# Kernel tuning notes

Hardware: AMD Instinct MI355X
Metric: run time of the kernel (lower is better)

The kernel has to match this reference:

```python
import jax, jax.numpy as jnp
import numpy as np

N = 100000        # nodes
E_HALF = 800000   # random edges before symmetrization
HID = 128         # hidden_dim
K = 4             # Chebyshev order
NEG = 0.01        # leaky_relu negative slope
BN_EPS = 1e-5
L2_EPS = 1e-12


def setup_inputs() -> dict:
    key = jax.random.key(0)
    ks = jax.random.split(key, 4)
    x = jax.random.normal(ks[0], (N, 3), dtype=jnp.float32)
    e = jax.random.randint(ks[1], (2, E_HALF), 0, N, dtype=jnp.int32)
    # symmetrize so the sym-normalized Laplacian is well defined
    edge_index = jnp.concatenate([e, e[::-1]], axis=1).astype(jnp.int64)

    def wcheb(k, fin, fout):
        return jax.random.normal(k, (K, fin, fout), dtype=jnp.float32) * np.float32(1.0 / np.sqrt(fin * K))

    wk = jax.random.split(ks[2], 5)
    return {
        "x": x, "edge_index": edge_index,
        "W1": wcheb(wk[0], 3, HID),   "b1": jnp.zeros((HID,), jnp.float32),
        "W2": wcheb(wk[1], HID, HID), "b2": jnp.zeros((HID,), jnp.float32),
        "W3": wcheb(wk[2], HID, HID), "b3": jnp.zeros((HID,), jnp.float32),
        "W4": wcheb(wk[3], HID, HID), "b4": jnp.zeros((HID,), jnp.float32),
        "g1": jnp.ones((HID,), jnp.float32), "be1": jnp.zeros((HID,), jnp.float32),
        "g2": jnp.ones((HID,), jnp.float32), "be2": jnp.zeros((HID,), jnp.float32),
        "g3": jnp.ones((HID,), jnp.float32), "be3": jnp.zeros((HID,), jnp.float32),
        "Wrep": jax.random.normal(wk[4], (HID, 3), dtype=jnp.float32) * np.float32(1.0 / np.sqrt(HID)),
        "brep": jnp.zeros((3,), jnp.float32),
    }


def _cheb(x, src, dst, norm, W, b):
    """PyG ChebConv (sym norm, lambda_max=2): out = sum_k T_k(L_hat) x @ W_k + b."""
    def prop(t):  # (L_hat t)_i = sum_{e: src->dst==i} norm_e * t[src_e]
        return jax.ops.segment_sum(t[src] * norm[:, None], dst, num_segments=N)
    Tx0 = x
    out = Tx0 @ W[0]
    Tx1 = prop(Tx0)
    out = out + Tx1 @ W[1]
    for k in range(2, W.shape[0]):
        Tx2 = 2.0 * prop(Tx1) - Tx0
        out = out + Tx2 @ W[k]
        Tx0, Tx1 = Tx1, Tx2
    return out + b


def _bn(x, g, b):  # BatchNorm1d, training mode (batch stats, biased var)
    mu = x.mean(axis=0)
    var = ((x - mu) ** 2).mean(axis=0)
    return (x - mu) * jax.lax.rsqrt(var + BN_EPS) * g + b


def _leaky(x):
    return jnp.where(x >= 0, x, NEG * x)


def reference(x, edge_index, W1, b1, W2, b2, W3, b3, W4, b4,
              g1, be1, g2, be2, g3, be3, Wrep, brep):
    src, dst = edge_index[0], edge_index[1]
    deg = jax.ops.segment_sum(jnp.ones(src.shape, jnp.float32), src, num_segments=N)
    dinv = jnp.where(deg > 0, jax.lax.rsqrt(jnp.maximum(deg, 1.0)), 0.0)
    # scaled Laplacian L_hat = -D^{-1/2} A D^{-1/2} (zero diagonal) for lambda_max=2
    norm = -(dinv[src] * dinv[dst])  # [E]

    h = _cheb(x.astype(jnp.float32), src, dst, norm, W1, b1)
    h = _bn(_leaky(h), g1, be1)
    h = _cheb(h, src, dst, norm, W2, b2)
    h = _bn(_leaky(h), g2, be2)
    h = _cheb(h, src, dst, norm, W3, b3)
    h = _bn(jnp.maximum(h, 0.0), g3, be3)
    h = _cheb(h, src, dst, norm, W4, b4)
    h = h / jnp.maximum(jnp.linalg.norm(h, axis=1, keepdims=True), L2_EPS)
    return h @ Wrep + brep  # [N, 3]
```

## Files before the change

### kernel.cpp

```cpp
#include <hip/hip_runtime.h>
#include <hip/hip_bf16.h>


#define HID 128
#define NEG 0.01f
#define BN_EPS 1e-5f
#define L2_EPS 1e-12f
#define CAP 64

typedef __attribute__((ext_vector_type(8))) short short8;
typedef __attribute__((ext_vector_type(4))) float floatx4;

__device__ __forceinline__ short f2bf(float f) {
    unsigned u = __float_as_uint(f);
    return (short)((u + 0x7fffu + ((u >> 16) & 1u)) >> 16);
}
__device__ __forceinline__ unsigned pack2bf(float x, float y) {
    return (unsigned)(unsigned short)f2bf(x) | ((unsigned)(unsigned short)f2bf(y) << 16);
}
__device__ __forceinline__ float bflo(unsigned u) { return __uint_as_float(u << 16); }
__device__ __forceinline__ float bfhi(unsigned u) { return __uint_as_float(u & 0xffff0000u); }
__device__ __forceinline__ float bf2f(unsigned short h) { return __uint_as_float((unsigned)h << 16); }

__device__ __forceinline__ float actf(float v, int act) {
    if (act == 0) return v >= 0.f ? v : NEG * v;
    if (act == 1) return v > 0.f ? v : 0.f;
    return v;
}


__global__ __launch_bounds__(256) void k_zero(int* __restrict__ arr, float* __restrict__ S, int N) {
    int i = blockIdx.x * 256 + threadIdx.x;
    if (i < N) arr[i * CAP] = 0;
    if (blockIdx.x == 0) {
        for (int k = threadIdx.x; k < 1024; k += 256) S[k] = 0.f;
    }
}

__global__ __launch_bounds__(256) void k_fillpad(const int* __restrict__ src, const int* __restrict__ dst,
                                                 int* __restrict__ arr, int E) {
    int e = blockIdx.x * 256 + threadIdx.x;
    if (e >= E) return;
    int d = dst[e];
    int pos = atomicAdd(&arr[d * CAP], 1);
    if (pos < CAP - 1) arr[d * CAP + 1 + pos] = src[e];
}

__global__ __launch_bounds__(256) void k_dinv(const int* __restrict__ arr, float* __restrict__ dinv,
                                              int* __restrict__ cnt, int N) {
    int i = blockIdx.x * 256 + threadIdx.x;
    if (i < N) {
        int d = arr[i * CAP];
        dinv[i] = d > 0 ? rsqrtf((float)d) : 0.f;
        cnt[i] = d < CAP - 1 ? d : CAP - 1;
    }
}

__global__ __launch_bounds__(256) void k_norm(const int* __restrict__ arr, const int* __restrict__ cnt,
                                              const float* __restrict__ dinv, int2* __restrict__ edges,
                                              float* __restrict__ snorm, int N) {
    int node = blockIdx.x * 4 + (threadIdx.x >> 6);
    if (node >= N) return;
    node = __builtin_amdgcn_readfirstlane(node);
    int lane = threadIdx.x & 63;
    int deg = cnt[node];
    float dd = dinv[node];
    int s = (lane < deg) ? arr[node * CAP + 1 + lane] : 0;
    float w = (lane < deg) ? -(dinv[s] * dd) : 0.f;
    if (lane < deg) {
        int2 rec;
        rec.x = s;
        rec.y = __float_as_int(w);
        edges[node * CAP + lane] = rec;
    }
    float sw = w;
    #pragma unroll
    for (int d = 1; d < 64; d <<= 1) sw += __shfl_xor(sw, d);
    if (lane == 0) snorm[node] = sw;
}


__global__ __launch_bounds__(256) void k_prop3(const float* __restrict__ T, const float* __restrict__ prev,
                                               float* __restrict__ out, const int* __restrict__ cnt,
                                               const int2* __restrict__ edges,
                                               float a, float b, int N) {
    int i = blockIdx.x * 256 + threadIdx.x;
    if (i >= N) return;
    float a0 = 0.f, a1 = 0.f, a2 = 0.f;
    int deg = cnt[i];
    int base = i * CAP;
    for (int j = 0; j < deg; ++j) {
        int2 r = edges[base + j];
        float w = __int_as_float(r.y);
        a0 += w * T[r.x * 3 + 0];
        a1 += w * T[r.x * 3 + 1];
        a2 += w * T[r.x * 3 + 2];
    }
    float r0 = a * a0, r1 = a * a1, r2 = a * a2;
    if (prev) {
        r0 += b * prev[i * 3 + 0];
        r1 += b * prev[i * 3 + 1];
        r2 += b * prev[i * 3 + 2];
    }
    out[i * 3 + 0] = r0;
    out[i * 3 + 1] = r1;
    out[i * 3 + 2] = r2;
}

__global__ __launch_bounds__(256, 8) void k_prop1(const unsigned* __restrict__ OUT,
                                                  unsigned* __restrict__ T1, unsigned* __restrict__ T0,
                                                  const int* __restrict__ cnt, const int2* __restrict__ edges,
                                                  const float* __restrict__ snorm, const float* __restrict__ S,
                                                  const float* __restrict__ g, const float* __restrict__ be,
                                                  int act, float invN, int N) {
    int lane = threadIdx.x & 63;
    int f0 = 2 * lane;
    float mu0 = S[f0] * invN, mu1 = S[f0 + 1] * invN;
    float v0 = S[f0 + 128] * invN - mu0 * mu0;
    float v1 = S[f0 + 129] * invN - mu1 * mu1;
    float a0 = g[f0] * rsqrtf(v0 + BN_EPS), a1 = g[f0 + 1] * rsqrtf(v1 + BN_EPS);
    float c0 = be[f0] - mu0 * a0, c1 = be[f0 + 1] - mu1 * a1;

    int wv = blockIdx.x * 4 + (threadIdx.x >> 6);
    int stride = gridDim.x * 4;
    for (int nv = wv; nv < N; nv += stride) {
        int node = __builtin_amdgcn_readfirstlane(nv);
        int deg = cnt[node];
        const int2* eb = edges + (size_t)node * CAP;
        float accx = 0.f, accy = 0.f;
        int j = 0;
        int nb = deg >> 3;
        if (nb > 0) {
            int2 recA[8]; unsigned tA[8];
            int2 recB[8]; unsigned tB[8];
            #pragma unroll
            for (int k = 0; k < 8; ++k) recA[k] = eb[k];
            #pragma unroll
            for (int k = 0; k < 8; ++k) tA[k] = OUT[(size_t)recA[k].x * 64 + lane];
            for (int bi = 1; bi < nb; ++bi) {
                const int2* ebb = eb + bi * 8;
                #pragma unroll
                for (int k = 0; k < 8; ++k) recB[k] = ebb[k];
                #pragma unroll
                for (int k = 0; k < 8; ++k) tB[k] = OUT[(size_t)recB[k].x * 64 + lane];
                #pragma unroll
                for (int k = 0; k < 8; ++k) {
                    float w = __int_as_float(recA[k].y);
                    accx += w * actf(bflo(tA[k]), act);
                    accy += w * actf(bfhi(tA[k]), act);
                }
                #pragma unroll
                for (int k = 0; k < 8; ++k) { recA[k] = recB[k]; tA[k] = tB[k]; }
            }
            #pragma unroll
            for (int k = 0; k < 8; ++k) {
                float w = __int_as_float(recA[k].y);
                accx += w * actf(bflo(tA[k]), act);
                accy += w * actf(bfhi(tA[k]), act);
            }
            j = nb * 8;
        }
        for (; j < deg; ++j) {
            int2 r = eb[j];
            float w = __int_as_float(r.y);
            unsigned t0 = OUT[(size_t)r.x * 64 + lane];
            accx += w * actf(bflo(t0), act);
            accy += w * actf(bfhi(t0), act);
        }
        float si = snorm[node];
        __builtin_nontemporal_store(pack2bf(a0 * accx + si * c0, a1 * accy + si * c1),
                                    &T1[(size_t)node * 64 + lane]);
        unsigned h = OUT[(size_t)node * 64 + lane];
        float t0lo = a0 * actf(bflo(h), act) + c0;
        float t0hi = a1 * actf(bfhi(h), act) + c1;
        __builtin_nontemporal_store(pack2bf(t0lo, t0hi), &T0[(size_t)node * 64 + lane]);
    }
}

__global__ __launch_bounds__(256, 8) void k_prop128(const unsigned* __restrict__ T, const unsigned* __restrict__ prev,
                                                    unsigned* __restrict__ out, const int* __restrict__ cnt,
                                                    const int2* __restrict__ edges,
                                                    float a, float b, int N) {
    int lane = threadIdx.x & 63;
    int wv = blockIdx.x * 4 + (threadIdx.x >> 6);
    int stride = gridDim.x * 4;
    for (int nv = wv; nv < N; nv += stride) {
        int node = __builtin_amdgcn_readfirstlane(nv);
        int deg = cnt[node];
        const int2* eb = edges + (size_t)node * CAP;
        float accx = 0.f, accy = 0.f;
        int j = 0;
        int nb = deg >> 3;
        if (nb > 0) {
            int2 recA[8]; unsigned tA[8];
            int2 recB[8]; unsigned tB[8];
            #pragma unroll
            for (int k = 0; k < 8; ++k) recA[k] = eb[k];
            #pragma unroll
            for (int k = 0; k < 8; ++k) tA[k] = T[(size_t)recA[k].x * 64 + lane];
            for (int bi = 1; bi < nb; ++bi) {
                const int2* ebb = eb + bi * 8;
                #pragma unroll
                for (int k = 0; k < 8; ++k) recB[k] = ebb[k];
                #pragma unroll
                for (int k = 0; k < 8; ++k) tB[k] = T[(size_t)recB[k].x * 64 + lane];
                #pragma unroll
                for (int k = 0; k < 8; ++k) {
                    float w = __int_as_float(recA[k].y);
                    accx += w * bflo(tA[k]);
                    accy += w * bfhi(tA[k]);
                }
                #pragma unroll
                for (int k = 0; k < 8; ++k) { recA[k] = recB[k]; tA[k] = tB[k]; }
            }
            #pragma unroll
            for (int k = 0; k < 8; ++k) {
                float w = __int_as_float(recA[k].y);
                accx += w * bflo(tA[k]);
                accy += w * bfhi(tA[k]);
            }
            j = nb * 8;
        }
        for (; j < deg; ++j) {
            int2 r = eb[j];
            float w = __int_as_float(r.y);
            unsigned t0 = T[(size_t)r.x * 64 + lane];
            accx += w * bflo(t0);
            accy += w * bfhi(t0);
        }
        float rx = a * accx, ry = a * accy;
        if (prev) {
            unsigned p = __builtin_nontemporal_load(&prev[(size_t)node * 64 + lane]);
            rx += b * bflo(p);
            ry += b * bfhi(p);
        }
        __builtin_nontemporal_store(pack2bf(rx, ry), &out[(size_t)node * 64 + lane]);
    }
}


__global__ __launch_bounds__(256) void k_gemm1(const float* __restrict__ x, const float* __restrict__ t1,
                                               const float* __restrict__ t2, const float* __restrict__ t3,
                                               const float* __restrict__ W, const float* __restrict__ b,
                                               unsigned short* __restrict__ OUT, float* __restrict__ S,
                                               int npb, int N) {
    __shared__ float Wl[12 * 128];
    __shared__ float bl[128];
    __shared__ float sS[256];
    int tid = threadIdx.x;
    for (int i = tid; i < 1536; i += 256) Wl[i] = W[i];
    if (tid < 128) bl[tid] = b[tid];
    if (tid < 256) sS[tid] = 0.f;
    __syncthreads();
    int f = tid & 127;
    int base = blockIdx.x * npb;
    int end = base + npb < N ? base + npb : N;
    const float* rows[4] = {x, t1, t2, t3};
    float s1 = 0.f, s2 = 0.f;
    for (int node = base + (tid >> 7); node < end; node += 2) {
        float acc = bl[f];
        #pragma unroll
        for (int k = 0; k < 4; ++k) {
            const float* r = rows[k] + (size_t)node * 3;
            acc += r[0] * Wl[(k * 3 + 0) * 128 + f];
            acc += r[1] * Wl[(k * 3 + 1) * 128 + f];
            acc += r[2] * Wl[(k * 3 + 2) * 128 + f];
        }
        unsigned short h = (unsigned short)f2bf(acc);
        OUT[(size_t)node * 128 + f] = h;
        float u = actf(bf2f(h), 0);
        s1 += u;
        s2 += u * u;
    }
    atomicAdd(&sS[f], s1);
    atomicAdd(&sS[f + 128], s2);
    __syncthreads();
    if (tid < 256) atomicAdd(&S[tid], sS[tid]);
}


__global__ __launch_bounds__(256) void k_packW(const float* __restrict__ WA, const float* __restrict__ WB,
                                               const float* __restrict__ WC, short* __restrict__ Wp) {
    int gid = blockIdx.x * 256 + threadIdx.x;
    int L = gid >> 16;
    int idx = gid & 65535;
    int j = idx & 7;
    int lane = (idx >> 3) & 63;
    int rest = idx >> 9;
    int nt = rest & 7;
    int ks = rest >> 3;
    int kk = ks * 32 + (lane >> 4) * 8 + j;
    int c = nt * 16 + (lane & 15);
    const float* W = (L == 0) ? WA : (L == 1) ? WB : WC;
    Wp[gid] = f2bf(W[(size_t)(kk >> 7) * 16384 + (kk & 127) * 128 + c]);
}

__global__ __launch_bounds__(512) void k_gemm512(const short* __restrict__ T0, const short* __restrict__ T1,
                                                 const short* __restrict__ T2, const short* __restrict__ T3,
                                                 const short* __restrict__ Wp, const float* __restrict__ bias,
                                                 unsigned short* __restrict__ OUT, float* __restrict__ S,
                                                 const float* __restrict__ Wrep, const float* __restrict__ brep,
                                                 float* __restrict__ fout,
                                                 int M, int doStats, int doFinal, int act) {
    __shared__ short Wlds[65536];
    __shared__ float sS[256];
    __shared__ float sW[388];
    int tid = threadIdx.x;
    int lane = tid & 63, wave = tid >> 6;
    if (tid < 256) sS[tid] = 0.f;
    if (doFinal) {
        for (int i = tid; i < 384; i += 512) sW[i] = Wrep[i];
        if (tid < 3) sW[384 + tid] = brep[tid];
    }
    for (int i = tid; i < 8192; i += 512) ((int4*)Wlds)[i] = ((const int4*)Wp)[i];
    __syncthreads();

    int quad = lane >> 4;
    int col0 = lane & 15;
    const short* Ts[4] = {T0, T1, T2, T3};
    float s1[8], s2[8];
    #pragma unroll
    for (int i = 0; i < 8; ++i) { s1[i] = 0.f; s2[i] = 0.f; }

    int nt32 = (M + 31) / 32;
    int stride = gridDim.x * 8;
    for (int t = blockIdx.x * 8 + wave; t < nt32; t += stride) {
        int r0 = t * 32;
        int rowa = r0 + col0;
        int rowb = rowa + 16;
        size_t rb0 = (size_t)(rowa < M ? rowa : M - 1) * 128;
        size_t rb1 = (size_t)(rowb < M ? rowb : M - 1) * 128;
        floatx4 acc0[8], acc1[8];
        #pragma unroll
        for (int i = 0; i < 8; ++i) {
            acc0[i][0] = 0.f; acc0[i][1] = 0.f; acc0[i][2] = 0.f; acc0[i][3] = 0.f;
            acc1[i][0] = 0.f; acc1[i][1] = 0.f; acc1[i][2] = 0.f; acc1[i][3] = 0.f;
        }
        #pragma unroll 4
        for (int ks = 0; ks < 16; ++ks) {
            const short* Tm = Ts[ks >> 2];
            int aoff = (ks & 3) * 32 + quad * 8;
            short8 af0 = *((const short8*)(Tm + rb0 + aoff));
            short8 af1 = *((const short8*)(Tm + rb1 + aoff));
            #pragma unroll
            for (int nt = 0; nt < 8; ++nt) {
                short8 bf = *((const short8*)(Wlds + ((ks * 8 + nt) * 64 + lane) * 8));
                acc0[nt] = __builtin_amdgcn_mfma_f32_16x16x32_bf16(af0, bf, acc0[nt], 0, 0, 0);
                acc1[nt] = __builtin_amdgcn_mfma_f32_16x16x32_bf16(af1, bf, acc1[nt], 0, 0, 0);
            }
        }
        if (doFinal) {
            #pragma unroll
            for (int half = 0; half < 2; ++half) {
                #pragma unroll
                for (int rg = 0; rg < 4; ++rg) {
                    int r = r0 + half * 16 + quad * 4 + rg;
                    float sq = 0.f, p0 = 0.f, p1 = 0.f, p2 = 0.f;
                    #pragma unroll
                    for (int nt = 0; nt < 8; ++nt) {
                        int c = nt * 16 + col0;
                        float v = (half ? acc1[nt][rg] : acc0[nt][rg]) + bias[c];
                        sq += v * v;
                        p0 += v * sW[c * 3 + 0];
                        p1 += v * sW[c * 3 + 1];
                        p2 += v * sW[c * 3 + 2];
                    }
                    #pragma unroll
                    for (int d = 1; d < 16; d <<= 1) {
                        sq += __shfl_xor(sq, d);
                        p0 += __shfl_xor(p0, d);
                        p1 += __shfl_xor(p1, d);
                        p2 += __shfl_xor(p2, d);
                    }
                    if (col0 == 0 && r < M) {
                        float inv = 1.f / fmaxf(sqrtf(sq), L2_EPS);
                        fout[r * 3 + 0] = p0 * inv + sW[384];
                        fout[r * 3 + 1] = p1 * inv + sW[385];
                        fout[r * 3 + 2] = p2 * inv + sW[386];
                    }
                }
            }
        } else {
            #pragma unroll
            for (int half = 0; half < 2; ++half) {
                int rbase = r0 + half * 16 + quad * 4;
                #pragma unroll
                for (int nt = 0; nt < 8; ++nt) {
                    int c = nt * 16 + col0;
                    float bv = bias[c];
                    #pragma unroll
                    for (int rg = 0; rg < 4; ++rg) {
                        int r = rbase + rg;
                        if (r < M) {
                            float v = (half ? acc1[nt][rg] : acc0[nt][rg]) + bv;
                            unsigned short h = (unsigned short)f2bf(v);
                            OUT[(size_t)r * 128 + c] = h;
                            float u = actf(bf2f(h), act);
                            s1[nt] += u;
                            s2[nt] += u * u;
                        }
                    }
                }
            }
        }
    }
    if (doStats) {
        #pragma unroll
        for (int nt = 0; nt < 8; ++nt) {
            int c = nt * 16 + col0;
            atomicAdd(&sS[c], s1[nt]);
            atomicAdd(&sS[c + 128], s2[nt]);
        }
        __syncthreads();
        if (tid < 256) atomicAdd(&S[tid], sS[tid]);
    }
}


extern "C" void kernel_launch(void* const* d_in, const int* in_sizes, int n_in,
                              void* d_out, int out_size, void* d_ws, size_t ws_size,
                              hipStream_t stream) {
    const int N = in_sizes[0] / 3;
    const int E = in_sizes[1] / 2;

    const float* x    = (const float*)d_in[0];
    const int*   ei   = (const int*)d_in[1];
    const int* esrc = ei;
    const int* edst = ei + E;
    const float* W1 = (const float*)d_in[2];  const float* b1 = (const float*)d_in[3];
    const float* W2 = (const float*)d_in[4];  const float* b2 = (const float*)d_in[5];
    const float* W3 = (const float*)d_in[6];  const float* b3 = (const float*)d_in[7];
    const float* W4 = (const float*)d_in[8];  const float* b4 = (const float*)d_in[9];
    const float* g1 = (const float*)d_in[10]; const float* be1 = (const float*)d_in[11];
    const float* g2 = (const float*)d_in[12]; const float* be2 = (const float*)d_in[13];
    const float* g3 = (const float*)d_in[14]; const float* be3 = (const float*)d_in[15];
    const float* Wrep = (const float*)d_in[16]; const float* brep = (const float*)d_in[17];
    float* out = (float*)d_out;

    char* w = (char*)d_ws;
    size_t off = 0;
    auto alloc = [&](size_t bytes) { size_t o = off; off = (off + bytes + 255) & ~(size_t)255; return o; };
    int*   arr    = (int*)(w + alloc((size_t)N * CAP * 4));
    int*   cnt    = (int*)(w + alloc((size_t)N * 4));
    float* dinv   = (float*)(w + alloc((size_t)N * 4));
    float* snorm  = (float*)(w + alloc((size_t)N * 4));
    int2*  edges  = (int2*)(w + alloc((size_t)N * CAP * 8));
    short* Wp     = (short*)(w + alloc(3 * 65536 * 2));
    float* S      = (float*)(w + alloc(4 * 256 * 4));
    float* t1f    = (float*)(w + alloc((size_t)N * 3 * 4));
    float* t2f    = (float*)(w + alloc((size_t)N * 3 * 4));
    float* t3f    = (float*)(w + alloc((size_t)N * 3 * 4));
    short* T0     = (short*)(w + alloc((size_t)N * 128 * 2));
    short* T1     = (short*)(w + alloc((size_t)N * 128 * 2));
    short* T2     = (short*)(w + alloc((size_t)N * 128 * 2));
    short* T3     = (short*)(w + alloc((size_t)N * 128 * 2));
    unsigned short* OUT = (unsigned short*)(w + alloc((size_t)N * 128 * 2));

    int gE = (E + 255) / 256;
    int gN = (N + 255) / 256;
    int gW = (N + 3) / 4;
    int gP = 2048;
    float invN = 1.f / (float)N;
    int npb = (N + 255) / 256;

    k_zero<<<gN, 256, 0, stream>>>(arr, S, N);
    k_fillpad<<<gE, 256, 0, stream>>>(esrc, edst, arr, E);
    k_dinv<<<gN, 256, 0, stream>>>(arr, dinv, cnt, N);
    k_norm<<<gW, 256, 0, stream>>>(arr, cnt, dinv, edges, snorm, N);
    k_packW<<<768, 256, 0, stream>>>(W2, W3, W4, Wp);

    k_prop3<<<gN, 256, 0, stream>>>(x, nullptr, t1f, cnt, edges, 1.f, 0.f, N);
    k_prop3<<<gN, 256, 0, stream>>>(t1f, x, t2f, cnt, edges, 2.f, -1.f, N);
    k_prop3<<<gN, 256, 0, stream>>>(t2f, t1f, t3f, cnt, edges, 2.f, -1.f, N);
    k_gemm1<<<256, 256, 0, stream>>>(x, t1f, t2f, t3f, W1, b1, OUT, S, npb, N);

    const float* bs[3]  = {b2, b3, b4};
    const float* gs[3]  = {g2, g3, nullptr};
    const float* bes[3] = {be2, be3, nullptr};
    int actsIn[3] = {0, 0, 1};
    int actsOut[3] = {0, 1, 2};

    for (int l = 0; l < 3; ++l) {
        float* Sin = S + (size_t)l * 256;
        float* Sout = S + (size_t)(l + 1) * 256;
        const float* gc = (l == 0) ? g1 : gs[l - 1];
        const float* bc = (l == 0) ? be1 : bes[l - 1];
        k_prop1<<<gP, 256, 0, stream>>>((const unsigned*)OUT, (unsigned*)T1, (unsigned*)T0,
                                        cnt, edges, snorm, Sin, gc, bc, actsIn[l], invN, N);
        k_prop128<<<gP, 256, 0, stream>>>((const unsigned*)T1, (const unsigned*)T0, (unsigned*)T2,
                                          cnt, edges, 2.f, -1.f, N);
        k_prop128<<<gP, 256, 0, stream>>>((const unsigned*)T2, (const unsigned*)T1, (unsigned*)T3,
                                          cnt, edges, 2.f, -1.f, N);
        k_gemm512<<<256, 512, 0, stream>>>(T0, T1, T2, T3, Wp + (size_t)l * 65536, bs[l], OUT, Sout,
                                           Wrep, brep, out, N,
                                           l < 2 ? 1 : 0, l == 2 ? 1 : 0, actsOut[l]);
    }
}
```

Baseline: 1.082 ms.

## Split wavefront into four 16-lane groups gathering separate edges with 16-byte loads

The propagation kernels now split each wavefront into four 16-lane groups. Each group handles a different edge of a 4-edge batch, and each lane loads a uint4 (8 bf16 features) instead of one 32-bit word. The partial sums are combined with cross-lane shuffles, and the edge list is padded to a multiple of 4 with zero-weight records so the batch loop needs no tail. This aims to cut serialized per-edge gather latency and raise bytes per load instruction. In exchange it adds shuffle reductions, leaves three quarters of the lanes idle in the epilogue, and reads padded edge slots.

```diff
diff --git a/kernel.cpp b/kernel.cpp
--- a/kernel.cpp
+++ b/kernel.cpp
@@ -64,10 +64,11 @@
     node = __builtin_amdgcn_readfirstlane(node);
     int lane = threadIdx.x & 63;
     int deg = cnt[node];
+    int deg4 = (deg + 3) & ~3;
     float dd = dinv[node];
     int s = (lane < deg) ? arr[node * CAP + 1 + lane] : 0;
     float w = (lane < deg) ? -(dinv[s] * dd) : 0.f;
-    if (lane < deg) {
+    if (lane < deg4) {
         int2 rec;
         rec.x = s;
         rec.y = __float_as_int(w);
@@ -107,134 +108,145 @@
     out[i * 3 + 2] = r2;
 }
 
-__global__ __launch_bounds__(256, 8) void k_prop1(const unsigned* __restrict__ OUT,
-                                                  unsigned* __restrict__ T1, unsigned* __restrict__ T0,
-                                                  const int* __restrict__ cnt, const int2* __restrict__ edges,
-                                                  const float* __restrict__ snorm, const float* __restrict__ S,
-                                                  const float* __restrict__ g, const float* __restrict__ be,
-                                                  int act, float invN, int N) {
+#define GATHER4_SELECT(r0, r1, r2, r3, sx, wv)                                   \
+    {                                                                            \
+        int s01 = (g & 1) ? r1.x : r0.x;                                         \
+        int s23 = (g & 1) ? r3.x : r2.x;                                         \
+        sx = (g & 2) ? s23 : s01;                                                \
+        int w01 = (g & 1) ? r1.y : r0.y;                                         \
+        int w23 = (g & 1) ? r3.y : r2.y;                                         \
+        wv = __int_as_float((g & 2) ? w23 : w01);                                \
+    }
+
+__global__ __launch_bounds__(256, 8) void k_prop128(const unsigned* __restrict__ T, const unsigned* __restrict__ prev,
+                                                    unsigned* __restrict__ out, const int* __restrict__ cnt,
+                                                    const int2* __restrict__ edges,
+                                                    float a, float b, int N) {
     int lane = threadIdx.x & 63;
-    int f0 = 2 * lane;
-    float mu0 = S[f0] * invN, mu1 = S[f0 + 1] * invN;
-    float v0 = S[f0 + 128] * invN - mu0 * mu0;
-    float v1 = S[f0 + 129] * invN - mu1 * mu1;
-    float a0 = g[f0] * rsqrtf(v0 + BN_EPS), a1 = g[f0 + 1] * rsqrtf(v1 + BN_EPS);
-    float c0 = be[f0] - mu0 * a0, c1 = be[f0 + 1] - mu1 * a1;
-
+    int g = lane >> 4, u = lane & 15;
     int wv = blockIdx.x * 4 + (threadIdx.x >> 6);
     int stride = gridDim.x * 4;
     for (int nv = wv; nv < N; nv += stride) {
         int node = __builtin_amdgcn_readfirstlane(nv);
         int deg = cnt[node];
         const int2* eb = edges + (size_t)node * CAP;
-        float accx = 0.f, accy = 0.f;
-        int j = 0;
-        int nb = deg >> 3;
-        if (nb > 0) {
-            int2 recA[8]; unsigned tA[8];
-            int2 recB[8]; unsigned tB[8];
+        float acc[8];
+        #pragma unroll
+        for (int k = 0; k < 8; ++k) acc[k] = 0.f;
+        int nb = (deg + 3) >> 2;
+        for (int bi = 0; bi < nb; ++bi) {
+            int2 r0 = eb[bi * 4 + 0], r1 = eb[bi * 4 + 1];
+            int2 r2 = eb[bi * 4 + 2], r3 = eb[bi * 4 + 3];
+            int sx; float w;
+            GATHER4_SELECT(r0, r1, r2, r3, sx, w);
+            uint4 t = *((const uint4*)(T + (size_t)sx * 64) + u);
+            acc[0] += w * bflo(t.x); acc[1] += w * bfhi(t.x);
+            acc[2] += w * bflo(t.y); acc[3] += w * bfhi(t.y);
+            acc[4] += w * bflo(t.z); acc[5] += w * bfhi(t.z);
+            acc[6] += w * bflo(t.w); acc[7] += w * bfhi(t.w);
+        }
+        #pragma unroll
+        for (int k = 0; k < 8; ++k) {
+            acc[k] += __shfl_xor(acc[k], 16);
+            acc[k] += __shfl_xor(acc[k], 32);
+        }
+        if (g == 0) {
+            float r[8];
             #pragma unroll
-            for (int k = 0; k < 8; ++k) recA[k] = eb[k];
-            #pragma unroll
-            for (int k = 0; k < 8; ++k) tA[k] = OUT[(size_t)recA[k].x * 64 + lane];
-            for (int bi = 1; bi < nb; ++bi) {
-                const int2* ebb = eb + bi * 8;
-                #pragma unroll
-                for (int k = 0; k < 8; ++k) recB[k] = ebb[k];
-                #pragma unroll
-                for (int k = 0; k < 8; ++k) tB[k] = OUT[(size_t)recB[k].x * 64 + lane];
-                #pragma unroll
-                for (int k = 0; k < 8; ++k) {
-                    float w = __int_as_float(recA[k].y);
-                    accx += w * actf(bflo(tA[k]), act);
-                    accy += w * actf(bfhi(tA[k]), act);
-                }
-                #pragma unroll
-                for (int k = 0; k < 8; ++k) { recA[k] = recB[k]; tA[k] = tB[k]; }
+            for (int k = 0; k < 8; ++k) r[k] = a * acc[k];
+            if (prev) {
+                uint4 p = *((const uint4*)(prev + (size_t)node * 64) + u);
+                r[0] += b * bflo(p.x); r[1] += b * bfhi(p.x);
+                r[2] += b * bflo(p.y); r[3] += b * bfhi(p.y);
+                r[4] += b * bflo(p.z); r[5] += b * bfhi(p.z);
+                r[6] += b * bflo(p.w); r[7] += b * bfhi(p.w);
             }
-            #pragma unroll
-            for (int k = 0; k < 8; ++k) {
-                float w = __int_as_float(recA[k].y);
-                accx += w * actf(bflo(tA[k]), act);
-                accy += w * actf(bfhi(tA[k]), act);
-            }
-            j = nb * 8;
-        }
-        for (; j < deg; ++j) {
-            int2 r = eb[j];
-            float w = __int_as_float(r.y);
-            unsigned t0 = OUT[(size_t)r.x * 64 + lane];
-            accx += w * actf(bflo(t0), act);
-            accy += w * actf(bfhi(t0), act);
-        }
-        float si = snorm[node];
-        __builtin_nontemporal_store(pack2bf(a0 * accx + si * c0, a1 * accy + si * c1),
-                                    &T1[(size_t)node * 64 + lane]);
-        unsigned h = OUT[(size_t)node * 64 + lane];
-        float t0lo = a0 * actf(bflo(h), act) + c0;
-        float t0hi = a1 * actf(bfhi(h), act) + c1;
-        __builtin_nontemporal_store(pack2bf(t0lo, t0hi), &T0[(size_t)node * 64 + lane]);
-    }
-}
-
-__global__ __launch_bounds__(256, 8) void k_prop128(const unsigned* __restrict__ T, const unsigned* __restrict__ prev,
-                                                    unsigned* __restrict__ out, const int* __restrict__ cnt,
-                                                    const int2* __restrict__ edges,
-                                                    float a, float b, int N) {
+            uint4 o;
+            o.x = pack2bf(r[0], r[1]);
+            o.y = pack2bf(r[2], r[3]);
+            o.z = pack2bf(r[4], r[5]);
+            o.w = pack2bf(r[6], r[7]);
+            *((uint4*)(out + (size_t)node * 64) + u) = o;
+        }
+    }
+}
+
+__global__ __launch_bounds__(256, 8) void k_prop1(const unsigned* __restrict__ OUT,
+                                                  unsigned* __restrict__ T1, unsigned* __restrict__ T0,
+                                                  const int* __restrict__ cnt, const int2* __restrict__ edges,
+                                                  const float* __restrict__ snorm, const float* __restrict__ S,
+                                                  const float* __restrict__ g_, const float* __restrict__ be,
+                                                  int act, float invN, int N) {
     int lane = threadIdx.x & 63;
+    int g = lane >> 4, u = lane & 15;
+    float af[8], cf[8];
+    {
+        int f0 = 8 * u;
+        #pragma unroll
+        for (int k = 0; k < 8; ++k) {
+            float mu = S[f0 + k] * invN;
+            float var = S[f0 + k + 128] * invN - mu * mu;
+            float aa = g_[f0 + k] * rsqrtf(var + BN_EPS);
+            af[k] = aa;
+            cf[k] = be[f0 + k] - mu * aa;
+        }
+    }
     int wv = blockIdx.x * 4 + (threadIdx.x >> 6);
     int stride = gridDim.x * 4;
     for (int nv = wv; nv < N; nv += stride) {
         int node = __builtin_amdgcn_readfirstlane(nv);
         int deg = cnt[node];
         const int2* eb = edges + (size_t)node * CAP;
-        float accx = 0.f, accy = 0.f;
-        int j = 0;
-        int nb = deg >> 3;
-        if (nb > 0) {
-            int2 recA[8]; unsigned tA[8];
-            int2 recB[8]; unsigned tB[8];
+        float acc[8];
+        #pragma unroll
+        for (int k = 0; k < 8; ++k) acc[k] = 0.f;
+        int nb = (deg + 3) >> 2;
+        for (int bi = 0; bi < nb; ++bi) {
+            int2 r0 = eb[bi * 4 + 0], r1 = eb[bi * 4 + 1];
+            int2 r2 = eb[bi * 4 + 2], r3 = eb[bi * 4 + 3];
+            int sx; float w;
+            GATHER4_SELECT(r0, r1, r2, r3, sx, w);
+            uint4 t = *((const uint4*)(OUT + (size_t)sx * 64) + u);
+            acc[0] += w * actf(bflo(t.x), act); acc[1] += w * actf(bfhi(t.x), act);
+            acc[2] += w * actf(bflo(t.y), act); acc[3] += w * actf(bfhi(t.y), act);
+            acc[4] += w * actf(bflo(t.z), act); acc[5] += w * actf(bfhi(t.z), act);
+            acc[6] += w * actf(bflo(t.w), act); acc[7] += w * actf(bfhi(t.w), act);
+        }
+        #pragma unroll
+        for (int k = 0; k < 8; ++k) {
+            acc[k] += __shfl_xor(acc[k], 16);
+            acc[k] += __shfl_xor(acc[k], 32);
+        }
+        if (g == 0) {
+            float si = snorm[node];
+            float r[8];
             #pragma unroll
-            for (int k = 0; k < 8; ++k) recA[k] = eb[k];
-            #pragma unroll
-            for (int k = 0; k < 8; ++k) tA[k] = T[(size_t)recA[k].x * 64 + lane];
-            for (int bi = 1; bi < nb; ++bi) {
-                const int2* ebb = eb + bi * 8;
-                #pragma unroll
-                for (int k = 0; k < 8; ++k) recB[k] = ebb[k];
-                #pragma unroll
-                for (int k = 0; k < 8; ++k) tB[k] = T[(size_t)recB[k].x * 64 + lane];
-                #pragma unroll
-                for (int k = 0; k < 8; ++k) {
-                    float w = __int_as_float(recA[k].y);
-                    accx += w * bflo(tA[k]);
-                    accy += w * bfhi(tA[k]);
-                }
-                #pragma unroll
-                for (int k = 0; k < 8; ++k) { recA[k] = recB[k]; tA[k] = tB[k]; }
-            }
-            #pragma unroll
-            for (int k = 0; k < 8; ++k) {
-                float w = __int_as_float(recA[k].y);
-                accx += w * bflo(tA[k]);
-                accy += w * bfhi(tA[k]);
-            }
-            j = nb * 8;
-        }
-        for (; j < deg; ++j) {
-            int2 r = eb[j];
-            float w = __int_as_float(r.y);
-            unsigned t0 = T[(size_t)r.x * 64 + lane];
-            accx += w * bflo(t0);
-            accy += w * bfhi(t0);
-        }
-        float rx = a * accx, ry = a * accy;
-        if (prev) {
-            unsigned p = __builtin_nontemporal_load(&prev[(size_t)node * 64 + lane]);
-            rx += b * bflo(p);
-            ry += b * bfhi(p);
-        }
-        __builtin_nontemporal_store(pack2bf(rx, ry), &out[(size_t)node * 64 + lane]);
+            for (int k = 0; k < 8; ++k) r[k] = af[k] * acc[k] + si * cf[k];
+            uint4 o;
+            o.x = pack2bf(r[0], r[1]);
+            o.y = pack2bf(r[2], r[3]);
+            o.z = pack2bf(r[4], r[5]);
+            o.w = pack2bf(r[6], r[7]);
+            *((uint4*)(T1 + (size_t)node * 64) + u) = o;
+        }
+        if (g == 1) {
+            uint4 h = *((const uint4*)(OUT + (size_t)node * 64) + u);
+            float r[8];
+            r[0] = af[0] * actf(bflo(h.x), act) + cf[0];
+            r[1] = af[1] * actf(bfhi(h.x), act) + cf[1];
+            r[2] = af[2] * actf(bflo(h.y), act) + cf[2];
+            r[3] = af[3] * actf(bfhi(h.y), act) + cf[3];
+            r[4] = af[4] * actf(bflo(h.z), act) + cf[4];
+            r[5] = af[5] * actf(bfhi(h.z), act) + cf[5];
+            r[6] = af[6] * actf(bflo(h.w), act) + cf[6];
+            r[7] = af[7] * actf(bfhi(h.w), act) + cf[7];
+            uint4 o;
+            o.x = pack2bf(r[0], r[1]);
+            o.y = pack2bf(r[2], r[3]);
+            o.z = pack2bf(r[4], r[5]);
+            o.w = pack2bf(r[6], r[7]);
+            *((uint4*)(T0 + (size_t)node * 64) + u) = o;
+        }
     }
 }
 
```

New measurement: 1.090 ms. No clear change (+0.7%).
